# Optimization experiments

Measured on AMD Instinct MI355X. Metric: run time of the kernel, lower is better.

Reference implementation:

```python
import jax, jax.numpy as jnp
import numpy as np

EMBED_DIM = 512
NUM_HEADS = 8
HEAD_DIM = EMBED_DIM // NUM_HEADS  # 64
LN_EPS = 1e-5
SEQ = 2048
BATCH = 2


def sparsemax(z):
    """Sparsemax over last axis: euclidean projection of each row onto the simplex."""
    K = z.shape[-1]
    z_sorted = -jnp.sort(-z, axis=-1)                      # descending
    z_cumsum = jnp.cumsum(z_sorted, axis=-1)
    r = jnp.arange(1, K + 1, dtype=z.dtype)
    support = r * z_sorted > (z_cumsum - 1.0)
    k_int = jnp.sum(support.astype(jnp.int32), axis=-1, keepdims=True)  # support size >= 1
    tau_sum = jnp.take_along_axis(z_cumsum, k_int - 1, axis=-1)
    tau = (tau_sum - 1.0) / k_int.astype(z.dtype)
    return jnp.maximum(z - tau, 0.0)


def layer_norm(x, eps=LN_EPS):
    # per-head pattern normalization over head_dim, no affine (normalize_pattern_affine=False)
    mu = jnp.mean(x, axis=-1, keepdims=True)
    var = jnp.mean(jnp.square(x - mu), axis=-1, keepdims=True)
    return (x - mu) * jax.lax.rsqrt(var + eps)


def setup_inputs() -> dict:
    key = jax.random.key(0)
    ks = jax.random.split(key, 6)
    E = EMBED_DIM
    return {
        "query": jax.random.normal(ks[0], (SEQ, BATCH, E), dtype=jnp.float32),
        "key": jax.random.normal(ks[1], (SEQ, BATCH, E), dtype=jnp.float32),
        "value": jax.random.normal(ks[2], (SEQ, BATCH, E), dtype=jnp.float32),
        "in_proj_weight": 0.02 * jax.random.normal(ks[3], (3 * E, E), dtype=jnp.float32),
        "in_proj_bias": jnp.zeros((3 * E,), dtype=jnp.float32),
        "out_proj_weight": 0.02 * jax.random.normal(ks[4], (E, E), dtype=jnp.float32),
        "out_proj_bias": jnp.zeros((E,), dtype=jnp.float32),
        "update_steps_max": 0,  # single association pass
    }


def reference(query, key, value, in_proj_weight, in_proj_bias,
              out_proj_weight, out_proj_bias, update_steps_max):
    L, B, E = query.shape
    S = key.shape[0]
    H, D = NUM_HEADS, HEAD_DIM
    wq, wk, wv = in_proj_weight[:E], in_proj_weight[E:2 * E], in_proj_weight[2 * E:]
    bq, bk, bv = in_proj_bias[:E], in_proj_bias[E:2 * E], in_proj_bias[2 * E:]
    # projections (torch Linear: x @ W.T + b)
    q = (query @ wq.T + bq).reshape(L, B, H, D)
    k = (key @ wk.T + bk).reshape(S, B, H, D)
    v = (value @ wv.T + bv).reshape(S, B, H, D)
    # pattern normalization (normalize_pattern=True, no affine), then attention scaling
    q = layer_norm(q) * (float(D) ** -0.5)
    k = layer_norm(k)
    v = layer_norm(v)
    # association scores [B, H, Lq, Lk]
    scores = jnp.einsum('ibhd,jbhd->bhij', q, k)
    attn = sparsemax(scores)  # sparse='sparsemax' activation over key axis
    out = jnp.einsum('bhij,jbhd->ibhd', attn, v).reshape(L, B, E)
    return out @ out_proj_weight.T + out_proj_bias
```

## Files before the change

### kernel.cpp

```cpp
#include <hip/hip_runtime.h>

#define SEQ   2048
#define BATCH 2
#define EMB   512
#define NH    8

typedef short bf16x8 __attribute__((ext_vector_type(8)));
typedef float f32x4  __attribute__((ext_vector_type(4)));
typedef unsigned short u16;

static __device__ __forceinline__ u16 f2bf(float f) {
    unsigned u = __float_as_uint(f);
    return (u16)((u + 0x7FFF + ((u >> 16) & 1)) >> 16);
}
static __device__ __forceinline__ float bf2f(u16 h) {
    return __uint_as_float((unsigned)h << 16);
}
static __device__ __forceinline__ unsigned cvtpk(float a, float b) {
    unsigned r;
    asm("v_cvt_pk_bf16_f32 %0, %1, %2" : "=v"(r) : "v"(a), "v"(b));
    return r;
}
static __device__ __forceinline__ void split8(const float* p, bf16x8& hi, bf16x8& lo) {
    const float4 f0 = *(const float4*)p;
    const float4 f1 = *(const float4*)(p + 4);
    const float fv[8] = {f0.x, f0.y, f0.z, f0.w, f1.x, f1.y, f1.z, f1.w};
    union { unsigned w[4]; bf16x8 v; } H, L;
#pragma unroll
    for (int q = 0; q < 4; ++q) {
        const float a = fv[2 * q], b = fv[2 * q + 1];
        const unsigned h = cvtpk(a, b);
        const float la = a - __uint_as_float(h << 16);
        const float lb = b - __uint_as_float(h & 0xFFFF0000u);
        H.w[q] = h;
        L.w[q] = cvtpk(la, lb);
    }
    hi = H.v; lo = L.v;
}

#define IW4 196608
#define W4  262144
__global__ __launch_bounds__(256) void convert_w(
    const float* __restrict__ ipw, const float* __restrict__ opw,
    u16* __restrict__ iwh, u16* __restrict__ iwl,
    u16* __restrict__ owh, u16* __restrict__ owl)
{
    const int f = blockIdx.x * 256 + threadIdx.x;
    if (f >= W4) return;
    const float* src; u16 *dh, *dl; int o;
    if (f < IW4) { src = ipw; dh = iwh; dl = iwl; o = f; }
    else         { src = opw; dh = owh; dl = owl; o = f - IW4; }
    const float4 x = ((const float4*)src)[o];
    ushort4 hi, lo;
    hi.x = f2bf(x.x); lo.x = f2bf(x.x - bf2f(hi.x));
    hi.y = f2bf(x.y); lo.y = f2bf(x.y - bf2f(hi.y));
    hi.z = f2bf(x.z); lo.z = f2bf(x.z - bf2f(hi.z));
    hi.w = f2bf(x.w); lo.w = f2bf(x.w - bf2f(hi.w));
    ((ushort4*)dh)[o] = hi;
    ((ushort4*)dl)[o] = lo;
}

__global__ __launch_bounds__(256, 4) void gemm_qkv_ln_mfma(
    const float* __restrict__ query, const float* __restrict__ key_in,
    const float* __restrict__ value,
    const u16* __restrict__ iwh, const u16* __restrict__ iwl,
    const float* __restrict__ ipb,
    u16* __restrict__ qhi, u16* __restrict__ qlo,
    u16* __restrict__ khi, u16* __restrict__ klo,
    u16* __restrict__ vth, u16* __restrict__ vtl)
{
    const int z = blockIdx.z;
    const float* Xf = (z == 0) ? query : (z == 1) ? key_in : value;
    u16* dh = (z == 0) ? qhi : khi;
    u16* dl = (z == 0) ? qlo : klo;
    const float scale = (z == 0) ? 0.125f : 1.0f;

    const int t0  = blockIdx.x * 128;
    const int h   = blockIdx.y;
    const int og0 = z * EMB + h * 64;

    const int tid = threadIdx.x;
    const int w   = tid >> 6;
    const int l   = tid & 63;
    const int c   = l & 15;
    const int g   = l >> 4;

    f32x4 acc[2][4];
#pragma unroll
    for (int mf = 0; mf < 2; ++mf)
#pragma unroll
        for (int nf = 0; nf < 4; ++nf) acc[mf][nf] = (f32x4){0.f, 0.f, 0.f, 0.f};

    const int arow0 = t0 + w * 32 + c;
#pragma unroll
    for (int ks = 0; ks < 16; ++ks) {
        const int k0 = ks * 32 + g * 8;
        bf16x8 ah[2], al[2], bh[4], bl[4];
#pragma unroll
        for (int mf = 0; mf < 2; ++mf)
            split8(&Xf[(size_t)(arow0 + mf * 16) * EMB + k0], ah[mf], al[mf]);
#pragma unroll
        for (int nf = 0; nf < 4; ++nf) {
            const size_t r = (size_t)(og0 + nf * 16 + c) * EMB + k0;
            bh[nf] = *(const bf16x8*)&iwh[r];
            bl[nf] = *(const bf16x8*)&iwl[r];
        }
#pragma unroll
        for (int mf = 0; mf < 2; ++mf)
#pragma unroll
            for (int nf = 0; nf < 4; ++nf) {
                f32x4 t = acc[mf][nf];
                t = __builtin_amdgcn_mfma_f32_16x16x32_bf16(ah[mf], bh[nf], t, 0, 0, 0);
                t = __builtin_amdgcn_mfma_f32_16x16x32_bf16(al[mf], bh[nf], t, 0, 0, 0);
                t = __builtin_amdgcn_mfma_f32_16x16x32_bf16(ah[mf], bl[nf], t, 0, 0, 0);
                acc[mf][nf] = t;
            }
    }

#pragma unroll
    for (int nf = 0; nf < 4; ++nf) {
        const float bj = ipb[og0 + nf * 16 + c];
#pragma unroll
        for (int mf = 0; mf < 2; ++mf)
#pragma unroll
            for (int j = 0; j < 4; ++j) acc[mf][nf][j] += bj;
    }

#pragma unroll
    for (int mf = 0; mf < 2; ++mf) {
        float mu[4], rs[4];
#pragma unroll
        for (int j = 0; j < 4; ++j) {
            float s = acc[mf][0][j] + acc[mf][1][j] + acc[mf][2][j] + acc[mf][3][j];
#pragma unroll
            for (int d = 1; d <= 8; d <<= 1) s += __shfl_xor(s, d);
            mu[j] = s * (1.0f / 64.0f);
        }
#pragma unroll
        for (int j = 0; j < 4; ++j) {
            float t = 0.f;
#pragma unroll
            for (int nf = 0; nf < 4; ++nf) {
                const float dv = acc[mf][nf][j] - mu[j];
                t += dv * dv;
            }
#pragma unroll
            for (int d = 1; d <= 8; d <<= 1) t += __shfl_xor(t, d);
            rs[j] = rsqrtf(t * (1.0f / 64.0f) + 1e-5f) * scale;
        }
#pragma unroll
        for (int j = 0; j < 4; ++j) {
            const int tg = t0 + w * 32 + mf * 16 + g * 4 + j;
            const int ii = tg >> 1;
            const int b  = tg & 1;
            const int bh_ = b * NH + h;
#pragma unroll
            for (int nf = 0; nf < 4; ++nf) {
                const float val = (acc[mf][nf][j] - mu[j]) * rs[j];
                const u16 hi = f2bf(val);
                const u16 lo = f2bf(val - bf2f(hi));
                if (z == 2) {
                    const size_t a = ((size_t)bh_ * 64 + nf * 16 + c) * SEQ + ii;
                    vth[a] = hi; vtl[a] = lo;
                } else {
                    const size_t a = ((size_t)bh_ * SEQ + ii) * 64 + nf * 16 + c;
                    dh[a] = hi; dl[a] = lo;
                }
            }
        }
    }
}

__global__ __launch_bounds__(512, 2) void attn_sparsemax_mfma(
    const u16* __restrict__ qhi, const u16* __restrict__ qlo,
    const u16* __restrict__ khi, const u16* __restrict__ klo,
    const u16* __restrict__ vth, const u16* __restrict__ vtl,
    u16* __restrict__ aoh, u16* __restrict__ aol)
{
    __shared__ float Opart[8][16][65];
    __shared__ float wred[8][32];
    __shared__ float wcnt[8][32];

    const int tid = threadIdx.x;
    const int w   = tid >> 6;
    const int l   = tid & 63;
    const int c   = l & 15;
    const int g   = l >> 4;

    const int wgid = blockIdx.x;
    const int xcd  = wgid & 7;
    const int idx  = wgid >> 3;
    const int bh   = xcd * 2 + (idx >> 6);
    const int q0   = (idx & 63) * 32;

    const size_t bhoff = (size_t)bh * SEQ * 64;
    const u16* qh = qhi + bhoff;
    const u16* ql = qlo + bhoff;
    const u16* kh = khi + bhoff;
    const u16* kl = klo + bhoff;
    const u16* vh_ = vth + bhoff;
    const u16* vl_ = vtl + bhoff;

    bf16x8 qhf[2][2], qlf[2][2];
#pragma unroll
    for (int nf = 0; nf < 2; ++nf)
#pragma unroll
        for (int kf = 0; kf < 2; ++kf) {
            const size_t a = (size_t)(q0 + nf * 16 + c) * 64 + kf * 32 + g * 8;
            qhf[nf][kf] = *(const bf16x8*)&qh[a];
            qlf[nf][kf] = *(const bf16x8*)&ql[a];
        }

    const int wbase = w * 256;
    f32x4 acc[16][2];
#pragma unroll
    for (int mf = 0; mf < 16; ++mf) {
        const size_t kr = (size_t)(wbase + mf * 16 + c) * 64 + g * 8;
        const bf16x8 kh0 = *(const bf16x8*)&kh[kr];
        const bf16x8 kh1 = *(const bf16x8*)&kh[kr + 32];
        const bf16x8 kl0 = *(const bf16x8*)&kl[kr];
        const bf16x8 kl1 = *(const bf16x8*)&kl[kr + 32];
#pragma unroll
        for (int nf = 0; nf < 2; ++nf) {
            f32x4 t = (f32x4){0.f, 0.f, 0.f, 0.f};
            t = __builtin_amdgcn_mfma_f32_16x16x32_bf16(kh0, qhf[nf][0], t, 0, 0, 0);
            t = __builtin_amdgcn_mfma_f32_16x16x32_bf16(kh1, qhf[nf][1], t, 0, 0, 0);
            t = __builtin_amdgcn_mfma_f32_16x16x32_bf16(kl0, qhf[nf][0], t, 0, 0, 0);
            t = __builtin_amdgcn_mfma_f32_16x16x32_bf16(kl1, qhf[nf][1], t, 0, 0, 0);
            t = __builtin_amdgcn_mfma_f32_16x16x32_bf16(kh0, qlf[nf][0], t, 0, 0, 0);
            t = __builtin_amdgcn_mfma_f32_16x16x32_bf16(kh1, qlf[nf][1], t, 0, 0, 0);
            acc[mf][nf] = t;
        }
    }

    float tau[2];
    {
        float mx[2];
#pragma unroll
        for (int nf = 0; nf < 2; ++nf) {
            float m = -1e30f;
#pragma unroll
            for (int mf = 0; mf < 16; ++mf)
#pragma unroll
                for (int r = 0; r < 4; ++r) m = fmaxf(m, acc[mf][nf][r]);
            m = fmaxf(m, __shfl_xor(m, 16));
            m = fmaxf(m, __shfl_xor(m, 32));
            mx[nf] = m;
        }
        if (g == 0) {
            wred[w][c]      = mx[0];
            wred[w][16 + c] = mx[1];
        }
    }
    __syncthreads();
#pragma unroll
    for (int nf = 0; nf < 2; ++nf) {
        float m = -1e30f;
#pragma unroll
        for (int ww = 0; ww < 8; ++ww) m = fmaxf(m, wred[ww][nf * 16 + c]);
        tau[nf] = m - 1.0f;
    }

    int cprev[2] = {-1, -1};
    for (int it = 0; it < 24; ++it) {
        __syncthreads();
        float sj[2], cj[2];
#pragma unroll
        for (int nf = 0; nf < 2; ++nf) {
            float s = 0.f, cn = 0.f;
#pragma unroll
            for (int mf = 0; mf < 16; ++mf)
#pragma unroll
                for (int r = 0; r < 4; ++r) {
                    const float v = acc[mf][nf][r];
                    if (v > tau[nf]) { s += v; cn += 1.f; }
                }
            s  += __shfl_xor(s, 16);  cn += __shfl_xor(cn, 16);
            s  += __shfl_xor(s, 32);  cn += __shfl_xor(cn, 32);
            sj[nf] = s; cj[nf] = cn;
        }
        if (g == 0) {
#pragma unroll
            for (int nf = 0; nf < 2; ++nf) {
                wred[w][nf * 16 + c] = sj[nf];
                wcnt[w][nf * 16 + c] = cj[nf];
            }
        }
        __syncthreads();
        int changed = 0;
#pragma unroll
        for (int nf = 0; nf < 2; ++nf) {
            float S = 0.f, C = 0.f;
#pragma unroll
            for (int ww = 0; ww < 8; ++ww) {
                S += wred[ww][nf * 16 + c];
                C += wcnt[ww][nf * 16 + c];
            }
            tau[nf] = (S - 1.0f) / C;
            const int Ci = (int)C;
            changed |= (Ci != cprev[nf]);
            cprev[nf] = Ci;
        }
        if (!__any(changed)) break;
    }

    const int a1 = ((2 * (g & 1)) * 16 + c) * 4;
    const int a2 = a1 + 64;
    const bool hi_half = (g >> 1);

    f32x4 Oacc[4][2];
#pragma unroll
    for (int mo = 0; mo < 4; ++mo)
#pragma unroll
        for (int nf = 0; nf < 2; ++nf) Oacc[mo][nf] = (f32x4){0.f, 0.f, 0.f, 0.f};

#pragma unroll
    for (int ks = 0; ks < 8; ++ks) {
        unsigned Ha[2][2], La[2][2], Hb[2][2], Lb[2][2];
#pragma unroll
        for (int m01 = 0; m01 < 2; ++m01) {
            const int mf = 2 * ks + m01;
#pragma unroll
            for (int nf = 0; nf < 2; ++nf) {
                const f32x4 s = acc[mf][nf];
                const float p0 = fmaxf(s[0] - tau[nf], 0.f);
                const float p1 = fmaxf(s[1] - tau[nf], 0.f);
                const float p2 = fmaxf(s[2] - tau[nf], 0.f);
                const float p3 = fmaxf(s[3] - tau[nf], 0.f);
                const unsigned h0 = cvtpk(p0, p1);
                const unsigned h1 = cvtpk(p2, p3);
                const unsigned l0 = cvtpk(p0 - __uint_as_float(h0 << 16),
                                          p1 - __uint_as_float(h0 & 0xFFFF0000u));
                const unsigned l1 = cvtpk(p2 - __uint_as_float(h1 << 16),
                                          p3 - __uint_as_float(h1 & 0xFFFF0000u));
                if (m01 == 0) { Ha[nf][0] = h0; Ha[nf][1] = h1; La[nf][0] = l0; La[nf][1] = l1; }
                else          { Hb[nf][0] = h0; Hb[nf][1] = h1; Lb[nf][0] = l0; Lb[nf][1] = l1; }
            }
        }
        bf16x8 Bhi[2], Blo[2];
#pragma unroll
        for (int nf = 0; nf < 2; ++nf) {
            union { int w4[4]; bf16x8 v; } BH, BL;
#pragma unroll
            for (int q = 0; q < 2; ++q) {
                const int ha = __builtin_amdgcn_ds_bpermute(a1, (int)Ha[nf][q]);
                const int hb = __builtin_amdgcn_ds_bpermute(a1, (int)Hb[nf][q]);
                BH.w4[q] = hi_half ? hb : ha;
                const int ha2 = __builtin_amdgcn_ds_bpermute(a2, (int)Ha[nf][q]);
                const int hb2 = __builtin_amdgcn_ds_bpermute(a2, (int)Hb[nf][q]);
                BH.w4[2 + q] = hi_half ? hb2 : ha2;
                const int la = __builtin_amdgcn_ds_bpermute(a1, (int)La[nf][q]);
                const int lb = __builtin_amdgcn_ds_bpermute(a1, (int)Lb[nf][q]);
                BL.w4[q] = hi_half ? lb : la;
                const int la2 = __builtin_amdgcn_ds_bpermute(a2, (int)La[nf][q]);
                const int lb2 = __builtin_amdgcn_ds_bpermute(a2, (int)Lb[nf][q]);
                BL.w4[2 + q] = hi_half ? lb2 : la2;
            }
            Bhi[nf] = BH.v; Blo[nf] = BL.v;
        }
#pragma unroll
        for (int mo = 0; mo < 4; ++mo) {
            const size_t va = (size_t)(mo * 16 + c) * SEQ + wbase + ks * 32 + g * 8;
            const bf16x8 vh = *(const bf16x8*)&vh_[va];
            const bf16x8 vl = *(const bf16x8*)&vl_[va];
#pragma unroll
            for (int nf = 0; nf < 2; ++nf) {
                f32x4 t = Oacc[mo][nf];
                t = __builtin_amdgcn_mfma_f32_16x16x32_bf16(vh, Bhi[nf], t, 0, 0, 0);
                t = __builtin_amdgcn_mfma_f32_16x16x32_bf16(vh, Blo[nf], t, 0, 0, 0);
                t = __builtin_amdgcn_mfma_f32_16x16x32_bf16(vl, Bhi[nf], t, 0, 0, 0);
                Oacc[mo][nf] = t;
            }
        }
    }

    const int b_ = bh >> 3, h_ = bh & 7;
#pragma unroll
    for (int nf = 0; nf < 2; ++nf) {
        if (nf) __syncthreads();
#pragma unroll
        for (int mo = 0; mo < 4; ++mo)
#pragma unroll
            for (int r = 0; r < 4; ++r)
                Opart[w][c][mo * 16 + 4 * g + r] = Oacc[mo][nf][r];
        __syncthreads();
#pragma unroll
        for (int p = 0; p < 2; ++p) {
            const int idx2 = p * 512 + tid;
            const int d = idx2 & 63;
            const int i = idx2 >> 6;
            float sv = 0.f;
#pragma unroll
            for (int ww = 0; ww < 8; ++ww) sv += Opart[ww][i][d];
            const int irow = q0 + nf * 16 + i;
            const size_t oa = (size_t)(irow * BATCH + b_) * EMB + h_ * 64 + d;
            const u16 hv = f2bf(sv);
            aoh[oa] = hv;
            aol[oa] = f2bf(sv - bf2f(hv));
        }
    }
}

__global__ __launch_bounds__(256, 4) void gemm_out_mfma(
    const u16* __restrict__ aoh, const u16* __restrict__ aol,
    const u16* __restrict__ owh, const u16* __restrict__ owl,
    const float* __restrict__ opb, float* __restrict__ out)
{
    const int t0 = blockIdx.x * 128;
    const int o0 = blockIdx.y * 64;

    const int tid = threadIdx.x;
    const int w   = tid >> 6;
    const int l   = tid & 63;
    const int c   = l & 15;
    const int g   = l >> 4;

    f32x4 acc[2][4];
#pragma unroll
    for (int mf = 0; mf < 2; ++mf)
#pragma unroll
        for (int nf = 0; nf < 4; ++nf) acc[mf][nf] = (f32x4){0.f, 0.f, 0.f, 0.f};

    const int arow0 = t0 + w * 32 + c;
#pragma unroll
    for (int ks = 0; ks < 16; ++ks) {
        const int k0 = ks * 32 + g * 8;
        bf16x8 ah[2], al[2], bh[4], bl[4];
#pragma unroll
        for (int mf = 0; mf < 2; ++mf) {
            const size_t r = (size_t)(arow0 + mf * 16) * EMB + k0;
            ah[mf] = *(const bf16x8*)&aoh[r];
            al[mf] = *(const bf16x8*)&aol[r];
        }
#pragma unroll
        for (int nf = 0; nf < 4; ++nf) {
            const size_t r = (size_t)(o0 + nf * 16 + c) * EMB + k0;
            bh[nf] = *(const bf16x8*)&owh[r];
            bl[nf] = *(const bf16x8*)&owl[r];
        }
#pragma unroll
        for (int mf = 0; mf < 2; ++mf)
#pragma unroll
            for (int nf = 0; nf < 4; ++nf) {
                f32x4 t = acc[mf][nf];
                t = __builtin_amdgcn_mfma_f32_16x16x32_bf16(ah[mf], bh[nf], t, 0, 0, 0);
                t = __builtin_amdgcn_mfma_f32_16x16x32_bf16(al[mf], bh[nf], t, 0, 0, 0);
                t = __builtin_amdgcn_mfma_f32_16x16x32_bf16(ah[mf], bl[nf], t, 0, 0, 0);
                acc[mf][nf] = t;
            }
    }

#pragma unroll
    for (int mf = 0; mf < 2; ++mf)
#pragma unroll
        for (int j = 0; j < 4; ++j) {
            const int tg = t0 + w * 32 + mf * 16 + g * 4 + j;
#pragma unroll
            for (int nf = 0; nf < 4; ++nf)
                out[(size_t)tg * EMB + o0 + nf * 16 + c] =
                    acc[mf][nf][j] + opb[o0 + nf * 16 + c];
        }
}

extern "C" void kernel_launch(void* const* d_in, const int* in_sizes, int n_in,
                              void* d_out, int out_size, void* d_ws, size_t ws_size,
                              hipStream_t stream)
{
    const float* query = (const float*)d_in[0];
    const float* key_  = (const float*)d_in[1];
    const float* value = (const float*)d_in[2];
    const float* ipw   = (const float*)d_in[3];
    const float* ipb   = (const float*)d_in[4];
    const float* opw   = (const float*)d_in[5];
    const float* opb   = (const float*)d_in[6];

    char* ws = (char*)d_ws;
    const size_t MB = 1024 * 1024;
    u16* qhi = (u16*)(ws + 0 * MB);
    u16* qlo = (u16*)(ws + 4 * MB);
    u16* khi = (u16*)(ws + 8 * MB);
    u16* klo = (u16*)(ws + 12 * MB);
    u16* vth = (u16*)(ws + 16 * MB);
    u16* vtl = (u16*)(ws + 20 * MB);
    u16* aoh = (u16*)(ws + 24 * MB);
    u16* aol = (u16*)(ws + 28 * MB);
    u16* iwh = (u16*)(ws + 32 * MB);
    u16* iwl = (u16*)(ws + 34 * MB);
    u16* owh = (u16*)(ws + 36 * MB);
    u16* owl = (u16*)(ws + 37 * MB);
    float* out = (float*)d_out;
    (void)ws_size; (void)in_sizes; (void)n_in; (void)out_size;

    convert_w<<<1024, 256, 0, stream>>>(ipw, opw, iwh, iwl, owh, owl);
    gemm_qkv_ln_mfma<<<dim3(32, 8, 3), 256, 0, stream>>>(
        query, key_, value, iwh, iwl, ipb, qhi, qlo, khi, klo, vth, vtl);
    attn_sparsemax_mfma<<<1024, 512, 0, stream>>>(
        qhi, qlo, khi, klo, vth, vtl, aoh, aol);
    gemm_out_mfma<<<dim3(32, 8), 256, 0, stream>>>(
        aoh, aol, owh, owl, opb, out);
}
```

Before: 377.6 us.

## Stage epilogues through LDS for coalesced stores and replace bpermute P transposes

The QKV projection epilogue now writes normalized values into shared memory and re-reads them so each thread emits packed 16-byte hi/lo bf16 stores, including the transposed V layout. The output GEMM likewise stages results in LDS and stores float4 rows. In the attention kernel, the probability-fragment transpose uses a small per-wave LDS staging buffer instead of many ds_bpermute calls, and the sparsemax reduction buffers are double-buffered so one barrier per iteration is dropped. The aim is to remove scattered 2-byte global stores and shuffle overhead, at the cost of extra LDS usage, which may lower occupancy.

```diff
diff --git a/kernel.cpp b/kernel.cpp
--- a/kernel.cpp
+++ b/kernel.cpp
@@ -8,6 +8,7 @@
 typedef short bf16x8 __attribute__((ext_vector_type(8)));
 typedef float f32x4  __attribute__((ext_vector_type(4)));
 typedef unsigned short u16;
+typedef unsigned long long u64;
 
 static __device__ __forceinline__ u16 f2bf(float f) {
     unsigned u = __float_as_uint(f);
@@ -69,10 +70,10 @@
     u16* __restrict__ khi, u16* __restrict__ klo,
     u16* __restrict__ vth, u16* __restrict__ vtl)
 {
+    __shared__ float Et[8704];
+
     const int z = blockIdx.z;
     const float* Xf = (z == 0) ? query : (z == 1) ? key_in : value;
-    u16* dh = (z == 0) ? qhi : khi;
-    u16* dl = (z == 0) ? qlo : klo;
     const float scale = (z == 0) ? 0.125f : 1.0f;
 
     const int t0  = blockIdx.x * 128;
@@ -150,23 +151,74 @@
         }
 #pragma unroll
         for (int j = 0; j < 4; ++j) {
-            const int tg = t0 + w * 32 + mf * 16 + g * 4 + j;
-            const int ii = tg >> 1;
-            const int b  = tg & 1;
-            const int bh_ = b * NH + h;
+            const int tl = w * 32 + mf * 16 + g * 4 + j;
 #pragma unroll
             for (int nf = 0; nf < 4; ++nf) {
                 const float val = (acc[mf][nf][j] - mu[j]) * rs[j];
-                const u16 hi = f2bf(val);
-                const u16 lo = f2bf(val - bf2f(hi));
-                if (z == 2) {
-                    const size_t a = ((size_t)bh_ * 64 + nf * 16 + c) * SEQ + ii;
-                    vth[a] = hi; vtl[a] = lo;
-                } else {
-                    const size_t a = ((size_t)bh_ * SEQ + ii) * 64 + nf * 16 + c;
-                    dh[a] = hi; dl[a] = lo;
+                const int o = nf * 16 + c;
+                if (z == 2) Et[o * 133 + tl] = val;
+                else        Et[tl * 68 + o]  = val;
+            }
+        }
+    }
+    __syncthreads();
+
+    const int part = tid & 7;
+    if (z < 2) {
+        u16* dh = (z == 0) ? qhi : khi;
+        u16* dl = (z == 0) ? qlo : klo;
+#pragma unroll
+        for (int p = 0; p < 8; ++p) {
+            const int seg = p * 32 + (tid >> 3);
+            const int tl  = seg & 127;
+            const int hl  = seg >> 7;
+            const float4 v0 = *(const float4*)&Et[tl * 68 + part * 8];
+            const float4 v1 = *(const float4*)&Et[tl * 68 + part * 8 + 4];
+            const float vv[8] = {v0.x, v0.y, v0.z, v0.w, v1.x, v1.y, v1.z, v1.w};
+            unsigned pk[4];
+#pragma unroll
+            for (int q = 0; q < 4; ++q) {
+                u16 ua, ub;
+                if (hl == 0) { ua = f2bf(vv[2*q]); ub = f2bf(vv[2*q+1]); }
+                else {
+                    const u16 ha = f2bf(vv[2*q]),  hb = f2bf(vv[2*q+1]);
+                    ua = f2bf(vv[2*q] - bf2f(ha)); ub = f2bf(vv[2*q+1] - bf2f(hb));
                 }
-            }
+                pk[q] = (unsigned)ua | ((unsigned)ub << 16);
+            }
+            const int bh_ = (tl & 1) * NH + h;
+            const int ii  = (t0 >> 1) + (tl >> 1);
+            u16* dst = hl ? dl : dh;
+            *(uint4*)&dst[((size_t)bh_ * SEQ + ii) * 64 + part * 8] =
+                make_uint4(pk[0], pk[1], pk[2], pk[3]);
+        }
+    } else {
+#pragma unroll
+        for (int p = 0; p < 8; ++p) {
+            const int seg  = p * 32 + (tid >> 3);
+            const int d    = seg & 63;
+            const int rest = seg >> 6;
+            const int b    = rest & 1;
+            const int hl   = rest >> 1;
+            float vv[8];
+#pragma unroll
+            for (int k = 0; k < 8; ++k)
+                vv[k] = Et[d * 133 + 2 * (part * 8 + k) + b];
+            unsigned pk[4];
+#pragma unroll
+            for (int q = 0; q < 4; ++q) {
+                u16 ua, ub;
+                if (hl == 0) { ua = f2bf(vv[2*q]); ub = f2bf(vv[2*q+1]); }
+                else {
+                    const u16 ha = f2bf(vv[2*q]),  hb = f2bf(vv[2*q+1]);
+                    ua = f2bf(vv[2*q] - bf2f(ha)); ub = f2bf(vv[2*q+1] - bf2f(hb));
+                }
+                pk[q] = (unsigned)ua | ((unsigned)ub << 16);
+            }
+            const int bh_ = b * NH + h;
+            u16* dst = hl ? vtl : vth;
+            *(uint4*)&dst[((size_t)bh_ * 64 + d) * SEQ + (t0 >> 1) + part * 8] =
+                make_uint4(pk[0], pk[1], pk[2], pk[3]);
         }
     }
 }
@@ -177,9 +229,10 @@
     const u16* __restrict__ vth, const u16* __restrict__ vtl,
     u16* __restrict__ aoh, u16* __restrict__ aol)
 {
-    __shared__ float Opart[8][16][65];
-    __shared__ float wred[8][32];
-    __shared__ float wcnt[8][32];
+    __shared__ float Opart[8][16][66];
+    __shared__ u16   Pst[8][2][16][40];
+    __shared__ float wred[2][8][32];
+    __shared__ float wcnt[2][8][32];
 
     const int tid = threadIdx.x;
     const int w   = tid >> 6;
@@ -194,10 +247,10 @@
     const int q0   = (idx & 63) * 32;
 
     const size_t bhoff = (size_t)bh * SEQ * 64;
-    const u16* qh = qhi + bhoff;
-    const u16* ql = qlo + bhoff;
-    const u16* kh = khi + bhoff;
-    const u16* kl = klo + bhoff;
+    const u16* qh  = qhi + bhoff;
+    const u16* ql  = qlo + bhoff;
+    const u16* kh  = khi + bhoff;
+    const u16* kl  = klo + bhoff;
     const u16* vh_ = vth + bhoff;
     const u16* vl_ = vtl + bhoff;
 
@@ -233,7 +286,6 @@
         }
     }
 
-    float tau[2];
     {
         float mx[2];
 #pragma unroll
@@ -247,23 +299,22 @@
             m = fmaxf(m, __shfl_xor(m, 32));
             mx[nf] = m;
         }
-        if (g == 0) {
-            wred[w][c]      = mx[0];
-            wred[w][16 + c] = mx[1];
-        }
+        if (g == 0) { wred[0][w][c] = mx[0]; wred[0][w][16 + c] = mx[1]; }
     }
     __syncthreads();
+
+    float tau[2];
 #pragma unroll
     for (int nf = 0; nf < 2; ++nf) {
         float m = -1e30f;
 #pragma unroll
-        for (int ww = 0; ww < 8; ++ww) m = fmaxf(m, wred[ww][nf * 16 + c]);
+        for (int ww = 0; ww < 8; ++ww) m = fmaxf(m, wred[0][ww][nf * 16 + c]);
         tau[nf] = m - 1.0f;
     }
 
     int cprev[2] = {-1, -1};
     for (int it = 0; it < 24; ++it) {
-        __syncthreads();
+        const int bs = (~it) & 1;
         float sj[2], cj[2];
 #pragma unroll
         for (int nf = 0; nf < 2; ++nf) {
@@ -280,11 +331,8 @@
             sj[nf] = s; cj[nf] = cn;
         }
         if (g == 0) {
-#pragma unroll
-            for (int nf = 0; nf < 2; ++nf) {
-                wred[w][nf * 16 + c] = sj[nf];
-                wcnt[w][nf * 16 + c] = cj[nf];
-            }
+            wred[bs][w][c]      = sj[0];  wred[bs][w][16 + c] = sj[1];
+            wcnt[bs][w][c]      = cj[0];  wcnt[bs][w][16 + c] = cj[1];
         }
         __syncthreads();
         int changed = 0;
@@ -293,8 +341,8 @@
             float S = 0.f, C = 0.f;
 #pragma unroll
             for (int ww = 0; ww < 8; ++ww) {
-                S += wred[ww][nf * 16 + c];
-                C += wcnt[ww][nf * 16 + c];
+                S += wred[bs][ww][nf * 16 + c];
+                C += wcnt[bs][ww][nf * 16 + c];
             }
             tau[nf] = (S - 1.0f) / C;
             const int Ci = (int)C;
@@ -304,10 +352,6 @@
         if (!__any(changed)) break;
     }
 
-    const int a1 = ((2 * (g & 1)) * 16 + c) * 4;
-    const int a2 = a1 + 64;
-    const bool hi_half = (g >> 1);
-
     f32x4 Oacc[4][2];
 #pragma unroll
     for (int mo = 0; mo < 4; ++mo)
@@ -316,13 +360,18 @@
 
 #pragma unroll
     for (int ks = 0; ks < 8; ++ks) {
-        unsigned Ha[2][2], La[2][2], Hb[2][2], Lb[2][2];
-#pragma unroll
-        for (int m01 = 0; m01 < 2; ++m01) {
-            const int mf = 2 * ks + m01;
-#pragma unroll
-            for (int nf = 0; nf < 2; ++nf) {
-                const f32x4 s = acc[mf][nf];
+        bf16x8 vh[4], vl[4];
+#pragma unroll
+        for (int mo = 0; mo < 4; ++mo) {
+            const size_t va = (size_t)(mo * 16 + c) * SEQ + wbase + ks * 32 + g * 8;
+            vh[mo] = *(const bf16x8*)&vh_[va];
+            vl[mo] = *(const bf16x8*)&vl_[va];
+        }
+#pragma unroll
+        for (int nf = 0; nf < 2; ++nf) {
+#pragma unroll
+            for (int m01 = 0; m01 < 2; ++m01) {
+                const f32x4 s = acc[2 * ks + m01][nf];
                 const float p0 = fmaxf(s[0] - tau[nf], 0.f);
                 const float p1 = fmaxf(s[1] - tau[nf], 0.f);
                 const float p2 = fmaxf(s[2] - tau[nf], 0.f);
@@ -333,42 +382,17 @@
                                           p1 - __uint_as_float(h0 & 0xFFFF0000u));
                 const unsigned l1 = cvtpk(p2 - __uint_as_float(h1 << 16),
                                           p3 - __uint_as_float(h1 & 0xFFFF0000u));
-                if (m01 == 0) { Ha[nf][0] = h0; Ha[nf][1] = h1; La[nf][0] = l0; La[nf][1] = l1; }
-                else          { Hb[nf][0] = h0; Hb[nf][1] = h1; Lb[nf][0] = l0; Lb[nf][1] = l1; }
-            }
-        }
-        bf16x8 Bhi[2], Blo[2];
-#pragma unroll
-        for (int nf = 0; nf < 2; ++nf) {
-            union { int w4[4]; bf16x8 v; } BH, BL;
-#pragma unroll
-            for (int q = 0; q < 2; ++q) {
-                const int ha = __builtin_amdgcn_ds_bpermute(a1, (int)Ha[nf][q]);
-                const int hb = __builtin_amdgcn_ds_bpermute(a1, (int)Hb[nf][q]);
-                BH.w4[q] = hi_half ? hb : ha;
-                const int ha2 = __builtin_amdgcn_ds_bpermute(a2, (int)Ha[nf][q]);
-                const int hb2 = __builtin_amdgcn_ds_bpermute(a2, (int)Hb[nf][q]);
-                BH.w4[2 + q] = hi_half ? hb2 : ha2;
-                const int la = __builtin_amdgcn_ds_bpermute(a1, (int)La[nf][q]);
-                const int lb = __builtin_amdgcn_ds_bpermute(a1, (int)Lb[nf][q]);
-                BL.w4[q] = hi_half ? lb : la;
-                const int la2 = __builtin_amdgcn_ds_bpermute(a2, (int)La[nf][q]);
-                const int lb2 = __builtin_amdgcn_ds_bpermute(a2, (int)Lb[nf][q]);
-                BL.w4[2 + q] = hi_half ? lb2 : la2;
-            }
-            Bhi[nf] = BH.v; Blo[nf] = BL.v;
-        }
-#pragma unroll
-        for (int mo = 0; mo < 4; ++mo) {
-            const size_t va = (size_t)(mo * 16 + c) * SEQ + wbase + ks * 32 + g * 8;
-            const bf16x8 vh = *(const bf16x8*)&vh_[va];
-            const bf16x8 vl = *(const bf16x8*)&vl_[va];
-#pragma unroll
-            for (int nf = 0; nf < 2; ++nf) {
+                *(u64*)&Pst[w][0][c][m01 * 16 + g * 4] = (u64)h0 | ((u64)h1 << 32);
+                *(u64*)&Pst[w][1][c][m01 * 16 + g * 4] = (u64)l0 | ((u64)l1 << 32);
+            }
+            const bf16x8 Bhi = *(const bf16x8*)&Pst[w][0][c][g * 8];
+            const bf16x8 Blo = *(const bf16x8*)&Pst[w][1][c][g * 8];
+#pragma unroll
+            for (int mo = 0; mo < 4; ++mo) {
                 f32x4 t = Oacc[mo][nf];
-                t = __builtin_amdgcn_mfma_f32_16x16x32_bf16(vh, Bhi[nf], t, 0, 0, 0);
-                t = __builtin_amdgcn_mfma_f32_16x16x32_bf16(vh, Blo[nf], t, 0, 0, 0);
-                t = __builtin_amdgcn_mfma_f32_16x16x32_bf16(vl, Bhi[nf], t, 0, 0, 0);
+                t = __builtin_amdgcn_mfma_f32_16x16x32_bf16(vh[mo], Bhi, t, 0, 0, 0);
+                t = __builtin_amdgcn_mfma_f32_16x16x32_bf16(vh[mo], Blo, t, 0, 0, 0);
+                t = __builtin_amdgcn_mfma_f32_16x16x32_bf16(vl[mo], Bhi, t, 0, 0, 0);
                 Oacc[mo][nf] = t;
             }
         }
@@ -406,6 +430,8 @@
     const u16* __restrict__ owh, const u16* __restrict__ owl,
     const float* __restrict__ opb, float* __restrict__ out)
 {
+    __shared__ float Et[128 * 68];
+
     const int t0 = blockIdx.x * 128;
     const int o0 = blockIdx.y * 64;
 
@@ -454,12 +480,20 @@
     for (int mf = 0; mf < 2; ++mf)
 #pragma unroll
         for (int j = 0; j < 4; ++j) {
-            const int tg = t0 + w * 32 + mf * 16 + g * 4 + j;
+            const int tl = w * 32 + mf * 16 + g * 4 + j;
 #pragma unroll
             for (int nf = 0; nf < 4; ++nf)
-                out[(size_t)tg * EMB + o0 + nf * 16 + c] =
-                    acc[mf][nf][j] + opb[o0 + nf * 16 + c];
-        }
+                Et[tl * 68 + nf * 16 + c] = acc[mf][nf][j] + opb[o0 + nf * 16 + c];
+        }
+    __syncthreads();
+
+    const int part = tid & 15;
+#pragma unroll
+    for (int p = 0; p < 8; ++p) {
+        const int row = p * 16 + (tid >> 4);
+        const float4 v = *(const float4*)&Et[row * 68 + part * 4];
+        *(float4*)&out[(size_t)(t0 + row) * EMB + o0 + part * 4] = v;
+    }
 }
 
 extern "C" void kernel_launch(void* const* d_in, const int* in_sizes, int n_in,
```

New measurement: 369.2 us. 1.02x faster.
